# Performance work log

Measured on AMD Instinct MI355X. Metric: run time of the kernel, lower is better.

## Reference

```python
import jax, jax.numpy as jnp
import numpy as np

HIDDEN = 1024
HEADS = 16
HEAD_DIM = HIDDEN // HEADS


def setup_inputs() -> dict:
    key = jax.random.key(0)
    ks = jax.random.split(key, 9)
    B, S = 2, 2048
    std = 1.0 / np.sqrt(HIDDEN)
    def lin(k):
        return jax.random.uniform(k, (HIDDEN, HIDDEN), jnp.float32, -std, std)
    def bias(k):
        return jax.random.uniform(k, (HIDDEN,), jnp.float32, -std, std)
    return {
        "x": jax.random.normal(ks[0], (B, S, HIDDEN), jnp.float32),
        "Wq": lin(ks[1]), "bq": bias(ks[2]),
        "Wk": lin(ks[3]), "bk": bias(ks[4]),
        "Wv": lin(ks[5]), "bv": bias(ks[6]),
        "Wo": lin(ks[7]), "bo": bias(ks[8]),
    }


def reference(x, Wq, bq, Wk, bk, Wv, bv, Wo, bo):
    B, S, _ = x.shape
    scale = HEAD_DIM ** -0.5
    # projections; weights stored as (in, out) so y = x @ W + b
    def split_heads(y):
        return y.reshape(B, S, HEADS, HEAD_DIM).transpose(0, 2, 1, 3)  # b h s d
    q = split_heads(x @ Wq + bq)
    k = split_heads(x @ Wk + bk)
    v = split_heads(x @ Wv + bv)
    # dense attention: full [B,H,S,S] score matrix, as in the original
    scores = jnp.einsum("bhsd,bhtd->bhst", q, k) * scale
    attn = jax.nn.softmax(scores, axis=-1)
    out = jnp.einsum("bhst,bhtd->bhsd", attn, v)
    out = out.transpose(0, 2, 1, 3).reshape(B, S, HIDDEN)
    return out @ Wo + bo
```

## Files before the change

kernel.cpp:

```cpp
#include <hip/hip_runtime.h>
#include <hip/hip_bf16.h>

typedef unsigned short u16;
typedef __bf16 bf16x8 __attribute__((ext_vector_type(8)));
typedef float f32x4 __attribute__((ext_vector_type(4)));
typedef float f32x16 __attribute__((ext_vector_type(16)));
typedef unsigned u32x2 __attribute__((ext_vector_type(2)));
typedef unsigned u32x4 __attribute__((ext_vector_type(4)));

#define HIDDEN 1024
#define NH 16
#define HD 64
#define BATCH 2
#define SEQ 2048
#define MTOT (BATCH*SEQ)
#define CEXP 0.18033688f

#if __has_builtin(__builtin_amdgcn_exp2f)
#define EXP2(x) __builtin_amdgcn_exp2f(x)
#else
#define EXP2(x) __builtin_exp2f(x)
#endif

__device__ __forceinline__ u16 f2bf(float f) {
  union { float f; unsigned u; } v; v.f = f;
  unsigned u = v.u;
  return (u16)((u + 0x7fffu + ((u >> 16) & 1u)) >> 16);
}

__device__ __forceinline__ unsigned pack2bf(float a, float b) {
  __hip_bfloat162 h = __float22bfloat162_rn(make_float2(a, b));
  unsigned u; __builtin_memcpy(&u, &h, 4); return u;
}

__device__ __forceinline__ void gload16(const u16* g, u16* l) {
  __builtin_amdgcn_global_load_lds((const __attribute__((address_space(1))) unsigned int*)g,
                                   (__attribute__((address_space(3))) unsigned int*)l, 16, 0, 0);
}

__global__ __launch_bounds__(256) void convert_x_kernel(const float* __restrict__ x,
                                                        u16* __restrict__ xb) {
  size_t i = ((size_t)blockIdx.x * 256 + threadIdx.x) * 4;
  float4 v = *(const float4*)(x + i);
  uint2 p;
  p.x = pack2bf(v.x, v.y);
  p.y = pack2bf(v.z, v.w);
  *(uint2*)(xb + i) = p;
}

__global__ __launch_bounds__(256) void transpose_w_kernel(const float* __restrict__ w0, const float* __restrict__ w1,
                                                          const float* __restrict__ w2, const float* __restrict__ w3,
                                                          u16* __restrict__ dqkv, u16* __restrict__ dwo) {
  __shared__ float t[32][33];
  int z = blockIdx.z;
  const float* src = (z==0) ? w0 : (z==1) ? w1 : (z==2) ? w2 : w3;
  u16* dst = (z < 3) ? (dqkv + (size_t)z * HIDDEN * HIDDEN) : dwo;
  int kb = blockIdx.x * 32, nb = blockIdx.y * 32;
  int tx = threadIdx.x & 31, ty = threadIdx.x >> 5;
  for (int r = ty; r < 32; r += 8) t[r][tx] = src[(size_t)(kb + r) * HIDDEN + nb + tx];
  __syncthreads();
  for (int r = ty; r < 32; r += 8) dst[(size_t)(nb + r) * HIDDEN + kb + tx] = f2bf(t[tx][r]);
}

__global__ __launch_bounds__(256) void transpose_v_kernel(const u16* __restrict__ qkv,
                                                          u16* __restrict__ vt) {
  __shared__ u16 t[32][33];
  int bh = blockIdx.z; int b = bh >> 4, h = bh & 15;
  int t0 = blockIdx.x * 32, d0 = blockIdx.y * 32;
  int tx = threadIdx.x & 31, ty = threadIdx.x >> 5;
  for (int r = ty; r < 32; r += 8)
    t[r][tx] = qkv[(size_t)(b*SEQ + t0 + r) * (3*HIDDEN) + 2*HIDDEN + h*HD + d0 + tx];
  __syncthreads();
  for (int r = ty; r < 32; r += 8)
    vt[(size_t)(bh*HD + d0 + r) * SEQ + t0 + tx] = t[tx][r];
}

template<int MODE, int MT>
__global__ __launch_bounds__(256) void gemm_bt(const u16* __restrict__ A, const u16* __restrict__ Bt,
                                               const float* __restrict__ b0, const float* __restrict__ b1,
                                               const float* __restrict__ b2,
                                               u16* __restrict__ Cq, float* __restrict__ Cf,
                                               int M, int N, int K) {
  constexpr int MF = MT / 32;
  __shared__ u16 As[MT*32];
  __shared__ u16 Bs[128*32];
  const int tid = threadIdx.x, lane = tid & 63, wv = tid >> 6;
  const int m0 = blockIdx.x * MT, n0 = blockIdx.y * 128;
  const int wm = (wv >> 1) * (MT/2), wn = (wv & 1) * 64;
  const int col = lane & 15, quad = lane >> 4;
  const int lr = lane >> 2, lk = (lane & 3) * 8;
  f32x4 acc[MF][4] = {};
  for (int k0 = 0; k0 < K; k0 += 32) {
    if constexpr (MT == 128) {
      gload16(&A[(size_t)(m0 + wv*32      + lr)*K + k0 + lk], &As[wv*1024]);
      gload16(&A[(size_t)(m0 + wv*32 + 16 + lr)*K + k0 + lk], &As[wv*1024 + 512]);
    } else {
      gload16(&A[(size_t)(m0 + wv*16      + lr)*K + k0 + lk], &As[wv*512]);
    }
    gload16(&Bt[(size_t)(n0 + wv*32      + lr)*K + k0 + lk], &Bs[wv*1024]);
    gload16(&Bt[(size_t)(n0 + wv*32 + 16 + lr)*K + k0 + lk], &Bs[wv*1024 + 512]);
    __syncthreads();
    bf16x8 af[MF], bfr[4];
    #pragma unroll
    for (int i = 0; i < MF; i++) af[i]  = *(const bf16x8*)&As[(wm + i*16 + col)*32 + quad*8];
    #pragma unroll
    for (int i = 0; i < 4; i++)  bfr[i] = *(const bf16x8*)&Bs[(wn + i*16 + col)*32 + quad*8];
    #pragma unroll
    for (int mi = 0; mi < MF; mi++)
      #pragma unroll
      for (int ni = 0; ni < 4; ni++)
        acc[mi][ni] = __builtin_amdgcn_mfma_f32_16x16x32_bf16(af[mi], bfr[ni], acc[mi][ni], 0, 0, 0);
    __syncthreads();
  }
  if constexpr (MODE == 0) {
    #pragma unroll
    for (int mi = 0; mi < MF; mi++)
      #pragma unroll
      for (int ni = 0; ni < 4; ni++) {
        int n = n0 + wn + ni*16 + col;
        float bias = b0[n];
        #pragma unroll
        for (int r = 0; r < 4; r++) {
          int m = m0 + wm + mi*16 + quad*4 + r;
          Cf[(size_t)m*N + n] = acc[mi][ni][r] + bias;
        }
      }
  } else {
    const int seg = n0 >> 10;
    const float* bias = (seg == 0) ? b0 : (seg == 1) ? b1 : b2;
    const float scl = (seg == 0) ? CEXP : 1.0f;
    #pragma unroll
    for (int mi = 0; mi < MF; mi++)
      #pragma unroll
      for (int ni = 0; ni < 4; ni++) {
        int n = n0 + wn + ni*16 + col;
        float bv = bias[n & (HIDDEN-1)];
        #pragma unroll
        for (int r = 0; r < 4; r++) {
          int m = m0 + wm + mi*16 + quad*4 + r;
          Cq[(size_t)m*N + n] = f2bf((acc[mi][ni][r] + bv) * scl);
        }
      }
  }
}

__global__ __launch_bounds__(256) void attn_kernel(const u16* __restrict__ qkv,
                                                   const u16* __restrict__ vt,
                                                   u16* __restrict__ ao) {
  __shared__ u16 Ks[2*64*72];
  __shared__ u16 Vs[2*64*72];
  const int tid = threadIdx.x, lane = tid & 63, wv = tid >> 6;
  const int qt = blockIdx.x, bh = blockIdx.y;
  const int b = bh >> 4, h = bh & 15;
  const int l31 = lane & 31, hl = lane >> 5;

  bf16x8 qf[4];
  {
    const u16* qrow = qkv + (size_t)(b*SEQ + qt*128 + wv*32 + l31)*(3*HIDDEN) + h*HD + hl*8;
    #pragma unroll
    for (int kk = 0; kk < 4; kk++) qf[kk] = *(const bf16x8*)(qrow + kk*16);
  }
  bf16x8 ones;
  #pragma unroll
  for (int i = 0; i < 8; i++) ones[i] = (__bf16)1.0f;

  f32x16 o[2] = {};
  f32x16 rs = {};

  const int r0 = tid >> 3, r1 = (tid >> 3) + 32, koS = (tid & 7) * 8;
  const u16* gK = qkv + (size_t)b*SEQ*(3*HIDDEN) + HIDDEN + (size_t)h*HD;
  const u16* gV = vt + (size_t)bh*HD*SEQ;
  uint4 pK0 = *(const uint4*)&gK[(size_t)r0*(3*HIDDEN) + koS];
  uint4 pK1 = *(const uint4*)&gK[(size_t)r1*(3*HIDDEN) + koS];
  uint4 pV0 = *(const uint4*)&gV[(size_t)r0*SEQ + koS];
  uint4 pV1 = *(const uint4*)&gV[(size_t)r1*SEQ + koS];

  for (int it = 0; it < SEQ/64; ++it) {
    const int cur = (it & 1) * 4608;
    *(uint4*)&Ks[cur + r0*72 + koS] = pK0;
    *(uint4*)&Ks[cur + r1*72 + koS] = pK1;
    *(uint4*)&Vs[cur + r0*72 + koS] = pV0;
    *(uint4*)&Vs[cur + r1*72 + koS] = pV1;
    __syncthreads();
    if (it < SEQ/64 - 1) {
      int t0 = (it + 1) * 64;
      pK0 = *(const uint4*)&gK[(size_t)(t0 + r0)*(3*HIDDEN) + koS];
      pK1 = *(const uint4*)&gK[(size_t)(t0 + r1)*(3*HIDDEN) + koS];
      pV0 = *(const uint4*)&gV[(size_t)r0*SEQ + t0 + koS];
      pV1 = *(const uint4*)&gV[(size_t)r1*SEQ + t0 + koS];
    }

    f32x16 s[2] = {};
    #pragma unroll
    for (int kk = 0; kk < 4; kk++) {
      #pragma unroll
      for (int tt = 0; tt < 2; tt++) {
        bf16x8 kf = *(const bf16x8*)&Ks[cur + (tt*32 + l31)*72 + kk*16 + hl*8];
        s[tt] = __builtin_amdgcn_mfma_f32_32x32x16_bf16(kf, qf[kk], s[tt], 0, 0, 0);
      }
    }

    #pragma unroll
    for (int tt = 0; tt < 2; tt++) {
      unsigned w[8];
      #pragma unroll
      for (int j = 0; j < 8; j++) {
        float p0 = EXP2(s[tt][2*j]);
        float p1 = EXP2(s[tt][2*j+1]);
        w[j] = pack2bf(p0, p1);
      }
      u32x2 r02 = __builtin_amdgcn_permlane32_swap(w[0], w[2], false, false);
      u32x2 r13 = __builtin_amdgcn_permlane32_swap(w[1], w[3], false, false);
      u32x2 r46 = __builtin_amdgcn_permlane32_swap(w[4], w[6], false, false);
      u32x2 r57 = __builtin_amdgcn_permlane32_swap(w[5], w[7], false, false);
      u32x4 c0, c1;
      c0.x = r02[0]; c0.y = r13[0]; c0.z = r02[1]; c0.w = r13[1];
      c1.x = r46[0]; c1.y = r57[0]; c1.z = r46[1]; c1.w = r57[1];
      bf16x8 pf0 = __builtin_bit_cast(bf16x8, c0);
      bf16x8 pf1 = __builtin_bit_cast(bf16x8, c1);

      #pragma unroll
      for (int mt = 0; mt < 2; mt++) {
        bf16x8 vf0 = *(const bf16x8*)&Vs[cur + (mt*32 + l31)*72 + tt*32 + hl*8];
        bf16x8 vf1 = *(const bf16x8*)&Vs[cur + (mt*32 + l31)*72 + tt*32 + 16 + hl*8];
        o[mt] = __builtin_amdgcn_mfma_f32_32x32x16_bf16(vf0, pf0, o[mt], 0, 0, 0);
        o[mt] = __builtin_amdgcn_mfma_f32_32x32x16_bf16(vf1, pf1, o[mt], 0, 0, 0);
      }
      rs = __builtin_amdgcn_mfma_f32_32x32x16_bf16(ones, pf0, rs, 0, 0, 0);
      rs = __builtin_amdgcn_mfma_f32_32x32x16_bf16(ones, pf1, rs, 0, 0, 0);
    }
  }

  float inv = 1.0f / rs[0];
  u16* aop = ao + (size_t)(b*SEQ + qt*128 + wv*32 + l31)*HIDDEN + h*HD + hl*4;
  #pragma unroll
  for (int mt = 0; mt < 2; mt++)
    #pragma unroll
    for (int a4 = 0; a4 < 4; a4++) {
      uint2 w2;
      w2.x = pack2bf(o[mt][4*a4+0]*inv, o[mt][4*a4+1]*inv);
      w2.y = pack2bf(o[mt][4*a4+2]*inv, o[mt][4*a4+3]*inv);
      *(uint2*)&aop[mt*32 + 8*a4] = w2;
    }
}

extern "C" void kernel_launch(void* const* d_in, const int* in_sizes, int n_in,
                              void* d_out, int out_size, void* d_ws, size_t ws_size,
                              hipStream_t stream) {
  const float* x  = (const float*)d_in[0];
  const float* Wq = (const float*)d_in[1];
  const float* bq = (const float*)d_in[2];
  const float* Wk = (const float*)d_in[3];
  const float* bk = (const float*)d_in[4];
  const float* Wv = (const float*)d_in[5];
  const float* bv = (const float*)d_in[6];
  const float* Wo = (const float*)d_in[7];
  const float* bo = (const float*)d_in[8];
  float* out = (float*)d_out;

  char* w = (char*)d_ws;
  u16* xb    = (u16*)w; w += (size_t)MTOT*HIDDEN*2;
  u16* wtqkv = (u16*)w; w += (size_t)3*HIDDEN*HIDDEN*2;
  u16* wto   = (u16*)w; w += (size_t)HIDDEN*HIDDEN*2;
  u16* qkvb  = (u16*)w; w += (size_t)MTOT*3*HIDDEN*2;
  u16* vtb   = (u16*)w; w += (size_t)BATCH*NH*HD*SEQ*2;
  u16* aob   = (u16*)w; w += (size_t)MTOT*HIDDEN*2;

  convert_x_kernel<<<(MTOT*HIDDEN)/1024, 256, 0, stream>>>(x, xb);
  transpose_w_kernel<<<dim3(32, 32, 4), 256, 0, stream>>>(Wq, Wk, Wv, Wo, wtqkv, wto);
  gemm_bt<1,128><<<dim3(32, 24), 256, 0, stream>>>(xb, wtqkv, bq, bk, bv, qkvb, nullptr, MTOT, 3*HIDDEN, HIDDEN);
  transpose_v_kernel<<<dim3(SEQ/32, 2, BATCH*NH), 256, 0, stream>>>(qkvb, vtb);
  attn_kernel<<<dim3(SEQ/128, BATCH*NH), 256, 0, stream>>>(qkvb, vtb, aob);
  gemm_bt<0,64><<<dim3(64, 8), 256, 0, stream>>>(aob, wto, bo, nullptr, nullptr, nullptr, out, MTOT, HIDDEN, HIDDEN);
}
```

Measured before the change: 130.5 us.

## Fuse V transpose into QKV GEMM epilogue and widen attention KV tile

The QKV GEMM epilogue now writes the V segment directly in transposed per-head layout, which removes the separate transpose_v kernel launch and its extra global round trip. The attention kernel processes 128 keys per iteration instead of 64, which halves the number of barriers and loop iterations at the cost of more shared memory and registers. The row-sum is now accumulated with scalar adds plus a cross-half shuffle instead of extra MFMAs against a ones vector. The transposed V stores are strided 8-byte writes, which may coalesce poorly.

```diff
diff --git a/kernel.cpp b/kernel.cpp
--- a/kernel.cpp
+++ b/kernel.cpp
@@ -15,6 +15,7 @@
 #define SEQ 2048
 #define MTOT (BATCH*SEQ)
 #define CEXP 0.18033688f
+#define KVB 128
 
 #if __has_builtin(__builtin_amdgcn_exp2f)
 #define EXP2(x) __builtin_amdgcn_exp2f(x)
@@ -62,24 +63,12 @@
   for (int r = ty; r < 32; r += 8) dst[(size_t)(nb + r) * HIDDEN + kb + tx] = f2bf(t[tx][r]);
 }
 
-__global__ __launch_bounds__(256) void transpose_v_kernel(const u16* __restrict__ qkv,
-                                                          u16* __restrict__ vt) {
-  __shared__ u16 t[32][33];
-  int bh = blockIdx.z; int b = bh >> 4, h = bh & 15;
-  int t0 = blockIdx.x * 32, d0 = blockIdx.y * 32;
-  int tx = threadIdx.x & 31, ty = threadIdx.x >> 5;
-  for (int r = ty; r < 32; r += 8)
-    t[r][tx] = qkv[(size_t)(b*SEQ + t0 + r) * (3*HIDDEN) + 2*HIDDEN + h*HD + d0 + tx];
-  __syncthreads();
-  for (int r = ty; r < 32; r += 8)
-    vt[(size_t)(bh*HD + d0 + r) * SEQ + t0 + tx] = t[tx][r];
-}
-
 template<int MODE, int MT>
 __global__ __launch_bounds__(256) void gemm_bt(const u16* __restrict__ A, const u16* __restrict__ Bt,
                                                const float* __restrict__ b0, const float* __restrict__ b1,
                                                const float* __restrict__ b2,
-                                               u16* __restrict__ Cq, float* __restrict__ Cf,
+                                               u16* __restrict__ Cq, u16* __restrict__ Cv,
+                                               float* __restrict__ Cf,
                                                int M, int N, int K) {
   constexpr int MF = MT / 32;
   __shared__ u16 As[MT*32];
@@ -127,28 +116,45 @@
       }
   } else {
     const int seg = n0 >> 10;
-    const float* bias = (seg == 0) ? b0 : (seg == 1) ? b1 : b2;
-    const float scl = (seg == 0) ? CEXP : 1.0f;
-    #pragma unroll
-    for (int mi = 0; mi < MF; mi++)
-      #pragma unroll
-      for (int ni = 0; ni < 4; ni++) {
-        int n = n0 + wn + ni*16 + col;
-        float bv = bias[n & (HIDDEN-1)];
+    if (seg < 2) {
+      const float* bias = (seg == 0) ? b0 : b1;
+      const float scl = (seg == 0) ? CEXP : 1.0f;
+      #pragma unroll
+      for (int mi = 0; mi < MF; mi++)
         #pragma unroll
-        for (int r = 0; r < 4; r++) {
-          int m = m0 + wm + mi*16 + quad*4 + r;
-          Cq[(size_t)m*N + n] = f2bf((acc[mi][ni][r] + bv) * scl);
+        for (int ni = 0; ni < 4; ni++) {
+          int n = n0 + wn + ni*16 + col;
+          float bv = bias[n & (HIDDEN-1)];
+          #pragma unroll
+          for (int r = 0; r < 4; r++) {
+            int m = m0 + wm + mi*16 + quad*4 + r;
+            Cq[(size_t)m*N + n] = f2bf((acc[mi][ni][r] + bv) * scl);
+          }
         }
-      }
+    } else {
+      const int bb = m0 >> 11;
+      #pragma unroll
+      for (int mi = 0; mi < MF; mi++)
+        #pragma unroll
+        for (int ni = 0; ni < 4; ni++) {
+          int local = (n0 + wn + ni*16 + col) & (HIDDEN-1);
+          int hh = local >> 6, dd = local & 63;
+          float bv = b2[local];
+          int t4 = (m0 + wm + mi*16 + quad*4) & (SEQ-1);
+          uint2 w2;
+          w2.x = pack2bf(acc[mi][ni][0] + bv, acc[mi][ni][1] + bv);
+          w2.y = pack2bf(acc[mi][ni][2] + bv, acc[mi][ni][3] + bv);
+          *(uint2*)&Cv[((size_t)((bb*NH + hh)*HD + dd))*SEQ + t4] = w2;
+        }
+    }
   }
 }
 
 __global__ __launch_bounds__(256) void attn_kernel(const u16* __restrict__ qkv,
                                                    const u16* __restrict__ vt,
                                                    u16* __restrict__ ao) {
-  __shared__ u16 Ks[2*64*72];
-  __shared__ u16 Vs[2*64*72];
+  __shared__ u16 Ks[2*KVB*72];
+  __shared__ u16 Vs[2*64*136];
   const int tid = threadIdx.x, lane = tid & 63, wv = tid >> 6;
   const int qt = blockIdx.x, bh = blockIdx.y;
   const int b = bh >> 4, h = bh & 15;
@@ -160,53 +166,56 @@
     #pragma unroll
     for (int kk = 0; kk < 4; kk++) qf[kk] = *(const bf16x8*)(qrow + kk*16);
   }
-  bf16x8 ones;
-  #pragma unroll
-  for (int i = 0; i < 8; i++) ones[i] = (__bf16)1.0f;
 
   f32x16 o[2] = {};
-  f32x16 rs = {};
-
-  const int r0 = tid >> 3, r1 = (tid >> 3) + 32, koS = (tid & 7) * 8;
+  float rs0 = 0.f, rs1 = 0.f;
+
+  const int rK = tid >> 3, koK = (tid & 7) * 8;
+  const int rV = tid >> 4, koV = (tid & 15) * 8;
   const u16* gK = qkv + (size_t)b*SEQ*(3*HIDDEN) + HIDDEN + (size_t)h*HD;
   const u16* gV = vt + (size_t)bh*HD*SEQ;
-  uint4 pK0 = *(const uint4*)&gK[(size_t)r0*(3*HIDDEN) + koS];
-  uint4 pK1 = *(const uint4*)&gK[(size_t)r1*(3*HIDDEN) + koS];
-  uint4 pV0 = *(const uint4*)&gV[(size_t)r0*SEQ + koS];
-  uint4 pV1 = *(const uint4*)&gV[(size_t)r1*SEQ + koS];
-
-  for (int it = 0; it < SEQ/64; ++it) {
-    const int cur = (it & 1) * 4608;
-    *(uint4*)&Ks[cur + r0*72 + koS] = pK0;
-    *(uint4*)&Ks[cur + r1*72 + koS] = pK1;
-    *(uint4*)&Vs[cur + r0*72 + koS] = pV0;
-    *(uint4*)&Vs[cur + r1*72 + koS] = pV1;
+  uint4 pK[4], pV[4];
+  #pragma unroll
+  for (int s4 = 0; s4 < 4; s4++) {
+    pK[s4] = *(const uint4*)&gK[(size_t)(rK + 32*s4)*(3*HIDDEN) + koK];
+    pV[s4] = *(const uint4*)&gV[(size_t)(rV + 16*s4)*SEQ + koV];
+  }
+
+  for (int it = 0; it < SEQ/KVB; ++it) {
+    const int curK = (it & 1) * (KVB*72);
+    const int curV = (it & 1) * (64*136);
+    #pragma unroll
+    for (int s4 = 0; s4 < 4; s4++) {
+      *(uint4*)&Ks[curK + (rK + 32*s4)*72 + koK] = pK[s4];
+      *(uint4*)&Vs[curV + (rV + 16*s4)*136 + koV] = pV[s4];
+    }
     __syncthreads();
-    if (it < SEQ/64 - 1) {
-      int t0 = (it + 1) * 64;
-      pK0 = *(const uint4*)&gK[(size_t)(t0 + r0)*(3*HIDDEN) + koS];
-      pK1 = *(const uint4*)&gK[(size_t)(t0 + r1)*(3*HIDDEN) + koS];
-      pV0 = *(const uint4*)&gV[(size_t)r0*SEQ + t0 + koS];
-      pV1 = *(const uint4*)&gV[(size_t)r1*SEQ + t0 + koS];
-    }
-
-    f32x16 s[2] = {};
-    #pragma unroll
-    for (int kk = 0; kk < 4; kk++) {
-      #pragma unroll
-      for (int tt = 0; tt < 2; tt++) {
-        bf16x8 kf = *(const bf16x8*)&Ks[cur + (tt*32 + l31)*72 + kk*16 + hl*8];
-        s[tt] = __builtin_amdgcn_mfma_f32_32x32x16_bf16(kf, qf[kk], s[tt], 0, 0, 0);
-      }
-    }
-
-    #pragma unroll
-    for (int tt = 0; tt < 2; tt++) {
+    if (it < SEQ/KVB - 1) {
+      int t0 = (it + 1) * KVB;
+      #pragma unroll
+      for (int s4 = 0; s4 < 4; s4++) {
+        pK[s4] = *(const uint4*)&gK[(size_t)(t0 + rK + 32*s4)*(3*HIDDEN) + koK];
+        pV[s4] = *(const uint4*)&gV[(size_t)(rV + 16*s4)*SEQ + t0 + koV];
+      }
+    }
+
+    f32x16 sc[4] = {};
+    #pragma unroll
+    for (int kk = 0; kk < 4; kk++)
+      #pragma unroll
+      for (int tt = 0; tt < 4; tt++) {
+        bf16x8 kf = *(const bf16x8*)&Ks[curK + (tt*32 + l31)*72 + kk*16 + hl*8];
+        sc[tt] = __builtin_amdgcn_mfma_f32_32x32x16_bf16(kf, qf[kk], sc[tt], 0, 0, 0);
+      }
+
+    #pragma unroll
+    for (int tt = 0; tt < 4; tt++) {
       unsigned w[8];
       #pragma unroll
       for (int j = 0; j < 8; j++) {
-        float p0 = EXP2(s[tt][2*j]);
-        float p1 = EXP2(s[tt][2*j+1]);
+        float p0 = EXP2(sc[tt][2*j]);
+        float p1 = EXP2(sc[tt][2*j+1]);
+        rs0 += p0; rs1 += p1;
         w[j] = pack2bf(p0, p1);
       }
       u32x2 r02 = __builtin_amdgcn_permlane32_swap(w[0], w[2], false, false);
@@ -221,17 +230,17 @@
 
       #pragma unroll
       for (int mt = 0; mt < 2; mt++) {
-        bf16x8 vf0 = *(const bf16x8*)&Vs[cur + (mt*32 + l31)*72 + tt*32 + hl*8];
-        bf16x8 vf1 = *(const bf16x8*)&Vs[cur + (mt*32 + l31)*72 + tt*32 + 16 + hl*8];
+        bf16x8 vf0 = *(const bf16x8*)&Vs[curV + (mt*32 + l31)*136 + tt*32 + hl*8];
+        bf16x8 vf1 = *(const bf16x8*)&Vs[curV + (mt*32 + l31)*136 + tt*32 + 16 + hl*8];
         o[mt] = __builtin_amdgcn_mfma_f32_32x32x16_bf16(vf0, pf0, o[mt], 0, 0, 0);
         o[mt] = __builtin_amdgcn_mfma_f32_32x32x16_bf16(vf1, pf1, o[mt], 0, 0, 0);
       }
-      rs = __builtin_amdgcn_mfma_f32_32x32x16_bf16(ones, pf0, rs, 0, 0, 0);
-      rs = __builtin_amdgcn_mfma_f32_32x32x16_bf16(ones, pf1, rs, 0, 0, 0);
-    }
-  }
-
-  float inv = 1.0f / rs[0];
+    }
+  }
+
+  float my = rs0 + rs1;
+  float inv = 1.0f / (my + __shfl_xor(my, 32, 64));
+
   u16* aop = ao + (size_t)(b*SEQ + qt*128 + wv*32 + l31)*HIDDEN + h*HD + hl*4;
   #pragma unroll
   for (int mt = 0; mt < 2; mt++)
@@ -268,8 +277,7 @@
 
   convert_x_kernel<<<(MTOT*HIDDEN)/1024, 256, 0, stream>>>(x, xb);
   transpose_w_kernel<<<dim3(32, 32, 4), 256, 0, stream>>>(Wq, Wk, Wv, Wo, wtqkv, wto);
-  gemm_bt<1,128><<<dim3(32, 24), 256, 0, stream>>>(xb, wtqkv, bq, bk, bv, qkvb, nullptr, MTOT, 3*HIDDEN, HIDDEN);
-  transpose_v_kernel<<<dim3(SEQ/32, 2, BATCH*NH), 256, 0, stream>>>(qkvb, vtb);
+  gemm_bt<1,128><<<dim3(32, 24), 256, 0, stream>>>(xb, wtqkv, bq, bk, bv, qkvb, vtb, nullptr, MTOT, 3*HIDDEN, HIDDEN);
   attn_kernel<<<dim3(SEQ/128, BATCH*NH), 256, 0, stream>>>(qkvb, vtb, aob);
-  gemm_bt<0,64><<<dim3(64, 8), 256, 0, stream>>>(aob, wto, bo, nullptr, nullptr, nullptr, out, MTOT, HIDDEN, HIDDEN);
-}
+  gemm_bt<0,64><<<dim3(64, 8), 256, 0, stream>>>(aob, wto, bo, nullptr, nullptr, nullptr, nullptr, out, MTOT, HIDDEN, HIDDEN);
+}
```

Measured after the change: 203.4 us. 55.8% more time.
